# Optimization experiments

Measured on AMD Instinct MI355X. Metric: run time of the kernel, lower is better.

The kernel has to match this reference:

```python
import jax, jax.numpy as jnp
import numpy as np

N_HEAD, BS, F_IN, F_OUT = 4, 8192, 64, 64
LEAKY_ALPHA = 0.2


def setup_inputs() -> dict:
    key = jax.random.key(0)
    k1, k2, k3, k4 = jax.random.split(key, 4)
    return {
        "h": jax.random.normal(k1, (BS, F_IN), dtype=jnp.float32),
        "w": jax.random.normal(k2, (N_HEAD, F_IN, F_OUT), dtype=jnp.float32) * (1.0 / np.sqrt(F_IN)),
        "a_src": jax.random.normal(k3, (N_HEAD, F_OUT, 1), dtype=jnp.float32) * (1.0 / np.sqrt(F_OUT)),
        "a_dst": jax.random.normal(k4, (N_HEAD, F_OUT, 1), dtype=jnp.float32) * (1.0 / np.sqrt(F_OUT)),
        "bias": jnp.zeros((F_OUT,), dtype=jnp.float32),
    }


def reference(h, w, a_src, a_dst, bias):
    # h: [bs, f_in] broadcast-matmul with w: [n_head, f_in, f_out] -> [n_head, bs, f_out]
    h_prime = jnp.einsum("bi,hio->hbo", h, w)
    attn_src = jnp.einsum("hbo,ho->hb", h_prime, a_src[..., 0])  # [n_head, bs]
    attn_dst = jnp.einsum("hbo,ho->hb", h_prime, a_dst[..., 0])  # [n_head, bs]
    # additive scores: [n_head, bs, bs]
    attn = attn_src[:, :, None] + attn_dst[:, None, :]
    attn = jnp.where(attn >= 0, attn, LEAKY_ALPHA * attn)  # leaky_relu(0.2)
    attn = jax.nn.softmax(attn, axis=-1)
    # dropout is identity at inference
    out = jnp.einsum("hbn,hno->hbo", attn, h_prime) + bias  # [n_head, bs, f_out]
    out = jnp.transpose(out, (1, 0, 2))  # [bs, n_head, f_out]
    return out.reshape(out.shape[0], -1)  # [bs, n_head*f_out]
```

## Files before the change

kernel.cpp:

```cpp
#include <hip/hip_runtime.h>
#include <stdio.h>

#define H 4
#define B 8192
#define F 64
#define ALPHA 0.2f
#define NB 4096
#define DMIN (-8.0f)
#define DSCALE 256.0f
#define TSZ 32
#define NTL (B / TSZ)
#define PELD 132

__device__ __forceinline__ int bucket_of(float x)
{
  int b = (int)((x - DMIN) * DSCALE);
  return min(max(b, 0), NB - 1);
}

__global__ __launch_bounds__(256) void k_hprime(
    const float* __restrict__ h, const float* __restrict__ w,
    const float* __restrict__ a_src, const float* __restrict__ a_dst,
    float* __restrict__ hp, float* __restrict__ s, float* __restrict__ d)
{
  int head = blockIdx.y;
  int row0 = blockIdx.x * 64;
  __shared__ float wl[F * F];
  __shared__ float hl[64 * F];
  const float4* wsrc = (const float4*)(w + (size_t)head * F * F);
  const float4* hsrc = (const float4*)(h + (size_t)row0 * F);
  float4* wl4 = (float4*)wl;
  float4* hl4 = (float4*)hl;
  for (int t = threadIdx.x; t < F * F / 4; t += 256) { wl4[t] = wsrc[t]; hl4[t] = hsrc[t]; }
  __syncthreads();
  int o  = threadIdx.x & 63;
  int rb = threadIdx.x >> 6;
  float as = a_src[head * F + o];
  float ad = a_dst[head * F + o];
  float acc[16];
#pragma unroll
  for (int rg = 0; rg < 16; ++rg) acc[rg] = 0.f;
#pragma unroll 16
  for (int i = 0; i < F; ++i) {
    float wv = wl[i * F + o];
#pragma unroll
    for (int rg = 0; rg < 16; ++rg)
      acc[rg] = fmaf(hl[(rg * 4 + rb) * F + i], wv, acc[rg]);
  }
#pragma unroll
  for (int rg = 0; rg < 16; ++rg) {
    int r = row0 + rg * 4 + rb;
    hp[((size_t)head * B + r) * F + o] = acc[rg];
    float vs = acc[rg] * as, vd = acc[rg] * ad;
#pragma unroll
    for (int off = 32; off; off >>= 1) { vs += __shfl_down(vs, off); vd += __shfl_down(vd, off); }
    if (o == 0) {
      s[(size_t)head * B + r] = vs;
      d[(size_t)head * B + r] = vd;
    }
  }
}

__global__ __launch_bounds__(1024) void k_hist_scan(
    const float* __restrict__ d, int* __restrict__ bstart, int* __restrict__ gcur)
{
  int head = blockIdx.x;
  int tid = threadIdx.x;
  __shared__ int hist[NB];
  __shared__ int wtot[16], woff[16];
#pragma unroll
  for (int t = 0; t < NB / 1024; ++t) hist[tid + t * 1024] = 0;
  __syncthreads();
  const float* dh = d + (size_t)head * B;
#pragma unroll
  for (int t = 0; t < B / 1024; ++t)
    atomicAdd(&hist[bucket_of(dh[tid + t * 1024])], 1);
  __syncthreads();
  int h0 = hist[4 * tid], h1 = hist[4 * tid + 1], h2 = hist[4 * tid + 2], h3 = hist[4 * tid + 3];
  int sum = h0 + h1 + h2 + h3;
  int lane = tid & 63, wid = tid >> 6;
  int run = sum;
#pragma unroll
  for (int off = 1; off < 64; off <<= 1) {
    int v = __shfl_up(run, off);
    if (lane >= off) run += v;
  }
  if (lane == 63) wtot[wid] = run;
  __syncthreads();
  if (tid < 16) {
    int off = 0;
    for (int j = 0; j < tid; ++j) off += wtot[j];
    woff[tid] = off;
  }
  __syncthreads();
  int excl = woff[wid] + run - sum;
  int base = head * (NB + 1) + 4 * tid;
  int gbase = head * NB + 4 * tid;
  int e0 = excl, e1 = e0 + h0, e2 = e1 + h1, e3 = e2 + h2;
  bstart[base] = e0; bstart[base + 1] = e1; bstart[base + 2] = e2; bstart[base + 3] = e3;
  gcur[gbase] = e0; gcur[gbase + 1] = e1; gcur[gbase + 2] = e2; gcur[gbase + 3] = e3;
  if (tid == 1023) bstart[head * (NB + 1) + NB] = e3 + h3;
}

__global__ __launch_bounds__(512) void k_scatter(
    const float* __restrict__ d, int* __restrict__ gcur,
    float* __restrict__ ds, int* __restrict__ is)
{
  int head = blockIdx.y;
  int i = blockIdx.x * 512 + threadIdx.x;
  float v = d[(size_t)head * B + i];
  int b = bucket_of(v);
  int pos = atomicAdd(&gcur[head * NB + b], 1);
  ds[(size_t)head * B + pos] = v;
  is[(size_t)head * B + pos] = i;
}

__global__ __launch_bounds__(256) void k_sort(
    const float* __restrict__ dsort, const int* __restrict__ isort,
    const int* __restrict__ bstart, float* __restrict__ ds2, int* __restrict__ js2)
{
  int head = blockIdx.y;
  int b = blockIdx.x * 4 + (threadIdx.x >> 6);
  int lane = threadIdx.x & 63;
  int k0 = bstart[head * (NB + 1) + b];
  int k1 = bstart[head * (NB + 1) + b + 1];
  const float* dh = dsort + (size_t)head * B;
  const int*   ih = isort + (size_t)head * B;
  for (int e = k0 + lane; e < k1; e += 64) {
    float dv = dh[e]; int iv = ih[e];
    int rank = 0;
    for (int k = k0; k < k1; ++k) {
      float d2 = dh[k]; int i2 = ih[k];
      rank += (d2 < dv) || (d2 == dv && i2 < iv);
    }
    ds2[(size_t)head * B + k0 + rank] = dv;
    js2[(size_t)head * B + k0 + rank] = iv;
  }
}

__global__ __launch_bounds__(256) void k_peA(
    const float* __restrict__ ds2, const int* __restrict__ js2,
    const float* __restrict__ hp, float* __restrict__ TS)
{
  int head = blockIdx.y;
  int tile = blockIdx.x * 4 + (threadIdx.x >> 6);
  int o = threadIdx.x & 63;
  const float* dsh = ds2 + (size_t)head * B;
  const int*   jsh = js2 + (size_t)head * B;
  const float* hph = hp + (size_t)head * B * F;
  float a1 = 0.f, a2 = 0.f, s1 = 0.f, s2 = 0.f;
#pragma unroll 8
  for (int j = 0; j < TSZ; ++j) {
    int k = tile * TSZ + j;
    float dv = dsh[k];
    float e1 = expf(dv), e2 = expf(ALPHA * dv);
    float hv = hph[(size_t)jsh[k] * F + o];
    a1 = fmaf(e1, hv, a1); a2 = fmaf(e2, hv, a2);
    s1 += e1; s2 += e2;
  }
  float* row = TS + ((size_t)head * NTL + tile) * PELD;
  row[o] = a1; row[64 + o] = a2;
  if (o == 0) { row[128] = s1; row[129] = s2; }
}

__global__ __launch_bounds__(64) void k_peB(
    float* __restrict__ TS, float* __restrict__ totals)
{
  int head = blockIdx.y;
  int c = blockIdx.x;
  int lane = threadIdx.x;
  float* base = TS + (size_t)head * NTL * PELD + c;
  int t0 = lane * 4;
  float v[4];
#pragma unroll
  for (int t = 0; t < 4; ++t) v[t] = base[(size_t)(t0 + t) * PELD];
  float sum = 0.f;
#pragma unroll
  for (int t = 0; t < 4; ++t) { sum += v[t]; v[t] = sum; }
  float run = sum;
#pragma unroll
  for (int off = 1; off < 64; off <<= 1) {
    float u = __shfl_up(run, off);
    if (lane >= off) run += u;
  }
  float excl = run - sum;
  if (lane == 63) totals[head * PELD + c] = run;
#pragma unroll
  for (int t = 0; t < 4; ++t)
    base[(size_t)(t0 + t) * PELD] = excl + (t == 0 ? 0.f : v[t - 1]);
}

__global__ __launch_bounds__(256) void k_peC(
    const float* __restrict__ ds2, const int* __restrict__ js2,
    const float* __restrict__ hp, const float* __restrict__ TS,
    float* __restrict__ PE)
{
  int head = blockIdx.y;
  int tile = blockIdx.x * 4 + (threadIdx.x >> 6);
  int o = threadIdx.x & 63;
  const float* dsh = ds2 + (size_t)head * B;
  const int*   jsh = js2 + (size_t)head * B;
  const float* hph = hp + (size_t)head * B * F;
  const float* trow = TS + ((size_t)head * NTL + tile) * PELD;
  float a1 = trow[o], a2 = trow[64 + o], s1 = trow[128], s2 = trow[129];
  for (int j = 0; j < TSZ; ++j) {
    int k = tile * TSZ + j;
    float* row = PE + ((size_t)head * B + k) * PELD;
    row[o] = a1; row[64 + o] = a2;
    if (o == 0) { row[128] = s1; row[129] = s2; }
    float dv = dsh[k];
    float e1 = expf(dv), e2 = expf(ALPHA * dv);
    float hv = hph[(size_t)jsh[k] * F + o];
    a1 = fmaf(e1, hv, a1); a2 = fmaf(e2, hv, a2);
    s1 += e1; s2 += e2;
  }
}

__global__ __launch_bounds__(256) void k_out(
    const float* __restrict__ s, const float* __restrict__ ds2,
    const float* __restrict__ PE, const float* __restrict__ totals,
    const int* __restrict__ bstart, const float* __restrict__ bias,
    float* __restrict__ out)
{
  int head = blockIdx.y;
  int i = blockIdx.x * 4 + (threadIdx.x >> 6);
  int o = threadIdx.x & 63;
  float si = s[(size_t)head * B + i];
  float t = -si;
  int q = bucket_of(t);
  int k  = bstart[head * (NB + 1) + q];
  int Eq = bstart[head * (NB + 1) + q + 1];
  const float* dsh = ds2 + (size_t)head * B;
  while (k < Eq && dsh[k] < t) ++k;
  const float* row = (k < B) ? (PE + ((size_t)head * B + k) * PELD)
                             : (totals + head * PELD);
  float pe1 = row[o], pe2 = row[64 + o], p1 = row[128], p2 = row[129];
  float TE1 = totals[head * PELD + o];
  float T1  = totals[head * PELD + 128];
  float e1f = expf(si), e2f = expf(ALPHA * si);
  float denom = e2f * p2 + e1f * (T1 - p1);
  float num   = e2f * pe2 + e1f * (TE1 - pe1);
  out[(size_t)i * (H * F) + head * F + o] = num / denom + bias[o];
}

extern "C" void kernel_launch(void* const* d_in, const int* in_sizes, int n_in,
                              void* d_out, int out_size, void* d_ws, size_t ws_size,
                              hipStream_t stream)
{
  const float* h     = (const float*)d_in[0];
  const float* w     = (const float*)d_in[1];
  const float* a_src = (const float*)d_in[2];
  const float* a_dst = (const float*)d_in[3];
  const float* bias  = (const float*)d_in[4];
  float* out = (float*)d_out;

  float* p = (float*)d_ws;
  float* hp     = p; p += (size_t)H * B * F;
  float* s      = p; p += H * B;
  float* dd     = p; p += H * B;
  float* dsort  = p; p += H * B;
  int*   isort  = (int*)p; p += H * B;
  float* ds2    = p; p += H * B;
  int*   js2    = (int*)p; p += H * B;
  float* PE     = p; p += (size_t)H * B * PELD;
  float* TS     = p; p += (size_t)H * NTL * PELD;
  float* totals = p; p += H * PELD;
  int* bstart   = (int*)p; p += H * (NB + 1);
  int* gcur     = (int*)p; p += H * NB;

  size_t need = (size_t)((char*)p - (char*)d_ws);
  if (ws_size < need) {
    fprintf(stderr, "kernel_launch: ws_size %zu < needed %zu\n", ws_size, need);
    return;
  }

  k_hprime<<<dim3(B / 64, H), 256, 0, stream>>>(h, w, a_src, a_dst, hp, s, dd);
  k_hist_scan<<<H, 1024, 0, stream>>>(dd, bstart, gcur);
  k_scatter<<<dim3(B / 512, H), 512, 0, stream>>>(dd, gcur, dsort, isort);
  k_sort<<<dim3(NB / 4, H), 256, 0, stream>>>(dsort, isort, bstart, ds2, js2);
  k_peA<<<dim3(NTL / 4, H), 256, 0, stream>>>(ds2, js2, hp, TS);
  k_peB<<<dim3(130, H), 64, 0, stream>>>(TS, totals);
  k_peC<<<dim3(NTL / 4, H), 256, 0, stream>>>(ds2, js2, hp, TS, PE);
  k_out<<<dim3(B / 4, H), 256, 0, stream>>>(s, ds2, PE, totals, bstart, bias, out);
}
```

Measured before the change: 79.86 us.

## Fuse histogram, scatter and bucket sort into one LDS kernel; fold tile scan into peC

Histogram, scan, scatter and the in-bucket rank sort now run in a single block per head. The keys and indices are staged in shared memory, which removes two kernel launches and the global dsort/isort round trips. The separate tile prefix-scan kernel is also dropped. Each peC block now sums the preceding tile totals itself, and the last tile writes the grand totals. That removes another launch, but it makes later blocks re-read up to the full TS array. The sort now runs on only 4 blocks, so it gives up parallelism and uses about 96KB of LDS per block.

Measured after the change: 99.08 us. +24.1%, slower.

```diff
diff --git a/kernel.cpp b/kernel.cpp
--- a/kernel.cpp
+++ b/kernel.cpp
@@ -61,20 +61,26 @@
   }
 }
 
-__global__ __launch_bounds__(1024) void k_hist_scan(
-    const float* __restrict__ d, int* __restrict__ bstart, int* __restrict__ gcur)
+__global__ __launch_bounds__(1024) void k_prep(
+    const float* __restrict__ d, int* __restrict__ bstart,
+    float* __restrict__ ds2, int* __restrict__ js2)
 {
   int head = blockIdx.x;
   int tid = threadIdx.x;
-  __shared__ int hist[NB];
+  __shared__ int   hist[NB];
+  __shared__ int   cur[NB];
+  __shared__ float dls[B];
+  __shared__ int   ils[B];
   __shared__ int wtot[16], woff[16];
+  const float* dh = d + (size_t)head * B;
+  float v[8];
+#pragma unroll
+  for (int t = 0; t < 8; ++t) v[t] = dh[tid + t * 1024];
 #pragma unroll
   for (int t = 0; t < NB / 1024; ++t) hist[tid + t * 1024] = 0;
   __syncthreads();
-  const float* dh = d + (size_t)head * B;
-#pragma unroll
-  for (int t = 0; t < B / 1024; ++t)
-    atomicAdd(&hist[bucket_of(dh[tid + t * 1024])], 1);
+#pragma unroll
+  for (int t = 0; t < 8; ++t) atomicAdd(&hist[bucket_of(v[t])], 1);
   __syncthreads();
   int h0 = hist[4 * tid], h1 = hist[4 * tid + 1], h2 = hist[4 * tid + 2], h3 = hist[4 * tid + 3];
   int sum = h0 + h1 + h2 + h3;
@@ -82,8 +88,8 @@
   int run = sum;
 #pragma unroll
   for (int off = 1; off < 64; off <<= 1) {
-    int v = __shfl_up(run, off);
-    if (lane >= off) run += v;
+    int u = __shfl_up(run, off);
+    if (lane >= off) run += u;
   }
   if (lane == 63) wtot[wid] = run;
   __syncthreads();
@@ -94,47 +100,36 @@
   }
   __syncthreads();
   int excl = woff[wid] + run - sum;
-  int base = head * (NB + 1) + 4 * tid;
-  int gbase = head * NB + 4 * tid;
   int e0 = excl, e1 = e0 + h0, e2 = e1 + h1, e3 = e2 + h2;
-  bstart[base] = e0; bstart[base + 1] = e1; bstart[base + 2] = e2; bstart[base + 3] = e3;
-  gcur[gbase] = e0; gcur[gbase + 1] = e1; gcur[gbase + 2] = e2; gcur[gbase + 3] = e3;
-  if (tid == 1023) bstart[head * (NB + 1) + NB] = e3 + h3;
-}
-
-__global__ __launch_bounds__(512) void k_scatter(
-    const float* __restrict__ d, int* __restrict__ gcur,
-    float* __restrict__ ds, int* __restrict__ is)
-{
-  int head = blockIdx.y;
-  int i = blockIdx.x * 512 + threadIdx.x;
-  float v = d[(size_t)head * B + i];
-  int b = bucket_of(v);
-  int pos = atomicAdd(&gcur[head * NB + b], 1);
-  ds[(size_t)head * B + pos] = v;
-  is[(size_t)head * B + pos] = i;
-}
-
-__global__ __launch_bounds__(256) void k_sort(
-    const float* __restrict__ dsort, const int* __restrict__ isort,
-    const int* __restrict__ bstart, float* __restrict__ ds2, int* __restrict__ js2)
-{
-  int head = blockIdx.y;
-  int b = blockIdx.x * 4 + (threadIdx.x >> 6);
-  int lane = threadIdx.x & 63;
-  int k0 = bstart[head * (NB + 1) + b];
-  int k1 = bstart[head * (NB + 1) + b + 1];
-  const float* dh = dsort + (size_t)head * B;
-  const int*   ih = isort + (size_t)head * B;
-  for (int e = k0 + lane; e < k1; e += 64) {
-    float dv = dh[e]; int iv = ih[e];
+  cur[4 * tid] = e0; cur[4 * tid + 1] = e1; cur[4 * tid + 2] = e2; cur[4 * tid + 3] = e3;
+  int bb = head * (NB + 1);
+  bstart[bb + 4 * tid] = e0; bstart[bb + 4 * tid + 1] = e1;
+  bstart[bb + 4 * tid + 2] = e2; bstart[bb + 4 * tid + 3] = e3;
+  if (tid == 1023) bstart[bb + NB] = e3 + h3;
+  __syncthreads();
+#pragma unroll
+  for (int t = 0; t < 8; ++t) {
+    int b = bucket_of(v[t]);
+    int pos = atomicAdd(&cur[b], 1);
+    dls[pos] = v[t];
+    ils[pos] = tid + t * 1024;
+  }
+  __syncthreads();
+  size_t gb = (size_t)head * B;
+#pragma unroll
+  for (int t = 0; t < 8; ++t) {
+    int e = tid + t * 1024;
+    float dv = dls[e]; int iv = ils[e];
+    int b = bucket_of(dv);
+    int k0 = b ? cur[b - 1] : 0;
+    int k1 = cur[b];
     int rank = 0;
     for (int k = k0; k < k1; ++k) {
-      float d2 = dh[k]; int i2 = ih[k];
+      float d2 = dls[k]; int i2 = ils[k];
       rank += (d2 < dv) || (d2 == dv && i2 < iv);
     }
-    ds2[(size_t)head * B + k0 + rank] = dv;
-    js2[(size_t)head * B + k0 + rank] = iv;
+    ds2[gb + k0 + rank] = dv;
+    js2[gb + k0 + rank] = iv;
   }
 }
 
@@ -163,46 +158,38 @@
   if (o == 0) { row[128] = s1; row[129] = s2; }
 }
 
-__global__ __launch_bounds__(64) void k_peB(
-    float* __restrict__ TS, float* __restrict__ totals)
-{
-  int head = blockIdx.y;
-  int c = blockIdx.x;
-  int lane = threadIdx.x;
-  float* base = TS + (size_t)head * NTL * PELD + c;
-  int t0 = lane * 4;
-  float v[4];
-#pragma unroll
-  for (int t = 0; t < 4; ++t) v[t] = base[(size_t)(t0 + t) * PELD];
-  float sum = 0.f;
-#pragma unroll
-  for (int t = 0; t < 4; ++t) { sum += v[t]; v[t] = sum; }
-  float run = sum;
-#pragma unroll
-  for (int off = 1; off < 64; off <<= 1) {
-    float u = __shfl_up(run, off);
-    if (lane >= off) run += u;
-  }
-  float excl = run - sum;
-  if (lane == 63) totals[head * PELD + c] = run;
-#pragma unroll
-  for (int t = 0; t < 4; ++t)
-    base[(size_t)(t0 + t) * PELD] = excl + (t == 0 ? 0.f : v[t - 1]);
-}
-
 __global__ __launch_bounds__(256) void k_peC(
     const float* __restrict__ ds2, const int* __restrict__ js2,
     const float* __restrict__ hp, const float* __restrict__ TS,
-    float* __restrict__ PE)
-{
-  int head = blockIdx.y;
-  int tile = blockIdx.x * 4 + (threadIdx.x >> 6);
-  int o = threadIdx.x & 63;
+    float* __restrict__ PE, float* __restrict__ totals)
+{
+  int head = blockIdx.y;
+  int t0 = blockIdx.x * 4;
+  int o = threadIdx.x & 63, wv = threadIdx.x >> 6;
+  __shared__ float chA[4][64], chB[4][64], chS[4][2];
+  const float* tsh = TS + (size_t)head * NTL * PELD;
+  int len = t0 / 4;
+  float a1 = 0.f, a2 = 0.f, s1 = 0.f, s2 = 0.f;
+  for (int t = wv * len; t < (wv + 1) * len; ++t) {
+    const float* r = tsh + (size_t)t * PELD;
+    a1 += r[o]; a2 += r[64 + o]; s1 += r[128]; s2 += r[129];
+  }
+  chA[wv][o] = a1; chB[wv][o] = a2;
+  if (o == 0) { chS[wv][0] = s1; chS[wv][1] = s2; }
+  __syncthreads();
+  a1 = 0.f; a2 = 0.f; s1 = 0.f; s2 = 0.f;
+#pragma unroll
+  for (int c = 0; c < 4; ++c) {
+    a1 += chA[c][o]; a2 += chB[c][o]; s1 += chS[c][0]; s2 += chS[c][1];
+  }
+  for (int t = t0; t < t0 + wv; ++t) {
+    const float* r = tsh + (size_t)t * PELD;
+    a1 += r[o]; a2 += r[64 + o]; s1 += r[128]; s2 += r[129];
+  }
+  int tile = t0 + wv;
   const float* dsh = ds2 + (size_t)head * B;
   const int*   jsh = js2 + (size_t)head * B;
   const float* hph = hp + (size_t)head * B * F;
-  const float* trow = TS + ((size_t)head * NTL + tile) * PELD;
-  float a1 = trow[o], a2 = trow[64 + o], s1 = trow[128], s2 = trow[129];
   for (int j = 0; j < TSZ; ++j) {
     int k = tile * TSZ + j;
     float* row = PE + ((size_t)head * B + k) * PELD;
@@ -213,6 +200,11 @@
     float hv = hph[(size_t)jsh[k] * F + o];
     a1 = fmaf(e1, hv, a1); a2 = fmaf(e2, hv, a2);
     s1 += e1; s2 += e2;
+  }
+  if (tile == NTL - 1) {
+    totals[head * PELD + o] = a1;
+    totals[head * PELD + 64 + o] = a2;
+    if (o == 0) { totals[head * PELD + 128] = s1; totals[head * PELD + 129] = s2; }
   }
 }
 
@@ -258,15 +250,12 @@
   float* hp     = p; p += (size_t)H * B * F;
   float* s      = p; p += H * B;
   float* dd     = p; p += H * B;
-  float* dsort  = p; p += H * B;
-  int*   isort  = (int*)p; p += H * B;
   float* ds2    = p; p += H * B;
   int*   js2    = (int*)p; p += H * B;
   float* PE     = p; p += (size_t)H * B * PELD;
   float* TS     = p; p += (size_t)H * NTL * PELD;
   float* totals = p; p += H * PELD;
   int* bstart   = (int*)p; p += H * (NB + 1);
-  int* gcur     = (int*)p; p += H * NB;
 
   size_t need = (size_t)((char*)p - (char*)d_ws);
   if (ws_size < need) {
@@ -275,11 +264,8 @@
   }
 
   k_hprime<<<dim3(B / 64, H), 256, 0, stream>>>(h, w, a_src, a_dst, hp, s, dd);
-  k_hist_scan<<<H, 1024, 0, stream>>>(dd, bstart, gcur);
-  k_scatter<<<dim3(B / 512, H), 512, 0, stream>>>(dd, gcur, dsort, isort);
-  k_sort<<<dim3(NB / 4, H), 256, 0, stream>>>(dsort, isort, bstart, ds2, js2);
+  k_prep<<<H, 1024, 0, stream>>>(dd, bstart, ds2, js2);
   k_peA<<<dim3(NTL / 4, H), 256, 0, stream>>>(ds2, js2, hp, TS);
-  k_peB<<<dim3(130, H), 64, 0, stream>>>(TS, totals);
-  k_peC<<<dim3(NTL / 4, H), 256, 0, stream>>>(ds2, js2, hp, TS, PE);
+  k_peC<<<dim3(NTL / 4, H), 256, 0, stream>>>(ds2, js2, hp, TS, PE, totals);
   k_out<<<dim3(B / 4, H), 256, 0, stream>>>(s, ds2, PE, totals, bstart, bias, out);
 }
```
